# Kernel tuning notes

Hardware: AMD Instinct MI355X
Metric: run time of the kernel (lower is better)

The kernel has to match this reference:

```python
import jax, jax.numpy as jnp
import numpy as np

N_NODES = 50000
N_EDGES = 800000


def _sage(x, src, dst, Wl, Wr, b, n):
    # PyG SAGEConv: lin_l(mean aggr of neighbors) + lin_r(x) (+ bias in lin_l)
    agg = jax.ops.segment_sum(x[src], dst, num_segments=n)
    cnt = jax.ops.segment_sum(jnp.ones((src.shape[0],), x.dtype), dst, num_segments=n)
    mean = agg / jnp.maximum(cnt, 1.0)[:, None]
    return mean @ Wl + x @ Wr + b


def _gat(x, src, dst, W, att_src, att_dst, b, n):
    H, C = att_src.shape
    h = (x @ W).reshape(n, H, C)                      # [N,H,C]
    a_s = jnp.sum(h * att_src, axis=-1)               # [N,H]
    a_d = jnp.sum(h * att_dst, axis=-1)               # [N,H]
    e = jax.nn.leaky_relu(a_s[src] + a_d[dst], 0.2)   # [E,H]
    m = jax.ops.segment_max(e, dst, num_segments=n)   # per-dst softmax (stable)
    ex = jnp.exp(e - m[dst])
    s = jax.ops.segment_sum(ex, dst, num_segments=n)
    alpha = ex / (s[dst] + 1e-16)                     # [E,H]
    out = jax.ops.segment_sum(h[src] * alpha[:, :, None], dst, num_segments=n)
    return out.reshape(n, H * C) + b


def setup_inputs() -> dict:
    key = jax.random.key(0)
    ks = jax.random.split(key, 16)
    F_IN, H1, GH, HEADS, H2, NC = 20, 256, 32, 4, 256, 5
    GOUT = GH * HEADS
    sc = 0.05
    return {
        "x": jax.random.normal(ks[0], (N_NODES, F_IN), jnp.float32),
        "edge_index": jax.random.randint(ks[1], (2, N_EDGES), 0, N_NODES, jnp.int32),
        "sage1_Wl": jax.random.normal(ks[2], (F_IN, H1), jnp.float32) * sc,
        "sage1_Wr": jax.random.normal(ks[3], (F_IN, H1), jnp.float32) * sc,
        "sage1_b": jnp.zeros((H1,), jnp.float32),
        "gat_W": jax.random.normal(ks[4], (H1, GOUT), jnp.float32) * sc,
        "gat_att_src": jax.random.normal(ks[5], (HEADS, GH), jnp.float32) * sc,
        "gat_att_dst": jax.random.normal(ks[6], (HEADS, GH), jnp.float32) * sc,
        "gat_b": jnp.zeros((GOUT,), jnp.float32),
        "sage2_Wl": jax.random.normal(ks[7], (GOUT, H2), jnp.float32) * sc,
        "sage2_Wr": jax.random.normal(ks[8], (GOUT, H2), jnp.float32) * sc,
        "sage2_b": jnp.zeros((H2,), jnp.float32),
        "cls_W": jax.random.normal(ks[9], (H2, NC), jnp.float32) * sc,
        "cls_b": jnp.zeros((NC,), jnp.float32),
    }


def reference(x, edge_index, sage1_Wl, sage1_Wr, sage1_b, gat_W, gat_att_src,
              gat_att_dst, gat_b, sage2_Wl, sage2_Wr, sage2_b, cls_W, cls_b):
    n = x.shape[0]
    src, dst = edge_index[0], edge_index[1]
    h = jax.nn.relu(_sage(x, src, dst, sage1_Wl, sage1_Wr, sage1_b, n))
    h = jax.nn.elu(_gat(h, src, dst, gat_W, gat_att_src, gat_att_dst, gat_b, n))
    h = jax.nn.relu(_sage(h, src, dst, sage2_Wl, sage2_Wr, sage2_b, n))
    return h @ cls_W + cls_b
```

## Files before the change

kernel.cpp:

```cpp
#include <hip/hip_runtime.h>
#include <math.h>

#define N_NODES 50000
#define N_EDGES 800000
#define TPB 256
#define NCHUNK ((N_NODES + 255) / 256)

typedef short s16x8 __attribute__((ext_vector_type(8)));
typedef float f32x4 __attribute__((ext_vector_type(4)));

__device__ __forceinline__ unsigned short f2bf(float f) {
    unsigned u = __float_as_uint(f);
    u += 0x7fffu + ((u >> 16) & 1u);
    return (unsigned short)(u >> 16);
}
__device__ __forceinline__ float bf2f(unsigned short h) {
    return __uint_as_float(((unsigned)h) << 16);
}

__global__ void wt_k(const float* __restrict__ W1, int K1,
                     const float* __restrict__ W2, int K2,
                     int NO, int Kp, unsigned short* __restrict__ Wt) {
    int idx = blockIdx.x * TPB + threadIdx.x;
    if (idx >= NO * Kp) return;
    int n = idx / Kp, k = idx - n * Kp;
    float v = 0.f;
    if (k < K1) v = W1[(size_t)k * NO + n];
    else if (k < K1 + K2) v = W2[(size_t)(k - K1) * NO + n];
    Wt[idx] = f2bf(v);
}

__global__ void cast_k(const float4* __restrict__ in4, ushort4* __restrict__ outb) {
    int idx = blockIdx.x * TPB + threadIdx.x;
    if (idx >= N_NODES * 32) return;
    float4 v = in4[idx];
    ushort4 b;
    b.x = f2bf(v.x); b.y = f2bf(v.y); b.z = f2bf(v.z); b.w = f2bf(v.w);
    outb[idx] = b;
}

template<int ACT>
__global__ void gemm_mfma(const float* __restrict__ A1, int K1,
                          const float* __restrict__ A2, int K2,
                          const unsigned short* __restrict__ Wt, int Kp,
                          const float* __restrict__ bias,
                          float* __restrict__ out, int NO) {
    constexpr int BM = 128, BK = 32, LDP = 40;
    __shared__ unsigned short sA[BM * LDP];
    __shared__ unsigned short sB[128 * LDP];
    const int K = K1 + K2;
    const int T = Kp / BK;
    const int tid = threadIdx.x;
    const int lane = tid & 63, wid = tid >> 6;
    const int wr = wid >> 1, wc = wid & 1;
    const int row0 = blockIdx.y * BM, col0 = blockIdx.x * 128;
    const int l15 = lane & 15, l4 = lane >> 4;
    f32x4 acc[4][4] = {};

    for (int t = 0; t < T; ++t) {
        __syncthreads();
#pragma unroll
        for (int j = 0; j < 4; ++j) {
            int e = tid + j * 256;
            int r = e >> 3, k4 = e & 7;
            int kg = t * BK + k4 * 4, mg = row0 + r;
            float4 v = {0.f, 0.f, 0.f, 0.f};
            if (mg < N_NODES) {
                if (kg < K1)     v = *(const float4*)&A1[(size_t)mg * K1 + kg];
                else if (kg < K) v = *(const float4*)&A2[(size_t)mg * K2 + (kg - K1)];
            }
            ushort4 b;
            b.x = f2bf(v.x); b.y = f2bf(v.y); b.z = f2bf(v.z); b.w = f2bf(v.w);
            *(ushort4*)&sA[r * LDP + k4 * 4] = b;
        }
#pragma unroll
        for (int j = 0; j < 2; ++j) {
            int e = tid + j * 256;
            int n = e >> 2, k8 = e & 3;
            int4 v = *(const int4*)&Wt[(size_t)(col0 + n) * Kp + t * BK + k8 * 8];
            *(int4*)&sB[n * LDP + k8 * 8] = v;
        }
        __syncthreads();
        s16x8 af[4], bfr[4];
#pragma unroll
        for (int i = 0; i < 4; ++i) {
            af[i]  = *(const s16x8*)&sA[(wr * 64 + i * 16 + l15) * LDP + l4 * 8];
            bfr[i] = *(const s16x8*)&sB[(wc * 64 + i * 16 + l15) * LDP + l4 * 8];
        }
#pragma unroll
        for (int mi = 0; mi < 4; ++mi)
#pragma unroll
            for (int ni = 0; ni < 4; ++ni)
                acc[mi][ni] = __builtin_amdgcn_mfma_f32_16x16x32_bf16(
                    af[mi], bfr[ni], acc[mi][ni], 0, 0, 0);
    }
#pragma unroll
    for (int mi = 0; mi < 4; ++mi) {
#pragma unroll
        for (int ni = 0; ni < 4; ++ni) {
            int col = col0 + wc * 64 + ni * 16 + l15;
            float bb = bias ? bias[col] : 0.f;
#pragma unroll
            for (int r = 0; r < 4; ++r) {
                int row = row0 + wr * 64 + mi * 16 + l4 * 4 + r;
                if (row < N_NODES) {
                    float v = acc[mi][ni][r] + bb;
                    if (ACT) v = fmaxf(v, 0.f);
                    out[(size_t)row * NO + col] = v;
                }
            }
        }
    }
}

template<int ACT>
__global__ void gemm_mfma_bf(const unsigned short* __restrict__ A1, int K1,
                             const unsigned short* __restrict__ A2, int K2,
                             const unsigned short* __restrict__ Wt, int Kp,
                             const float* __restrict__ bias,
                             float* __restrict__ out, int NO) {
    constexpr int BM = 128, BK = 32, LDP = 40;
    __shared__ unsigned short sA[BM * LDP];
    __shared__ unsigned short sB[128 * LDP];
    const int T = Kp / BK;
    const int tid = threadIdx.x;
    const int lane = tid & 63, wid = tid >> 6;
    const int wr = wid >> 1, wc = wid & 1;
    const int row0 = blockIdx.y * BM, col0 = blockIdx.x * 128;
    const int l15 = lane & 15, l4 = lane >> 4;
    f32x4 acc[4][4] = {};

    for (int t = 0; t < T; ++t) {
        __syncthreads();
#pragma unroll
        for (int j = 0; j < 2; ++j) {
            int e = tid + j * 256;
            int r = e >> 2, k8 = e & 3;
            int kg = t * BK + k8 * 8, mg = row0 + r;
            int4 v = {0, 0, 0, 0};
            if (mg < N_NODES) {
                if (kg < K1) v = *(const int4*)&A1[(size_t)mg * K1 + kg];
                else         v = *(const int4*)&A2[(size_t)mg * K2 + (kg - K1)];
            }
            *(int4*)&sA[r * LDP + k8 * 8] = v;
        }
#pragma unroll
        for (int j = 0; j < 2; ++j) {
            int e = tid + j * 256;
            int n = e >> 2, k8 = e & 3;
            int4 v = *(const int4*)&Wt[(size_t)(col0 + n) * Kp + t * BK + k8 * 8];
            *(int4*)&sB[n * LDP + k8 * 8] = v;
        }
        __syncthreads();
        s16x8 af[4], bfr[4];
#pragma unroll
        for (int i = 0; i < 4; ++i) {
            af[i]  = *(const s16x8*)&sA[(wr * 64 + i * 16 + l15) * LDP + l4 * 8];
            bfr[i] = *(const s16x8*)&sB[(wc * 64 + i * 16 + l15) * LDP + l4 * 8];
        }
#pragma unroll
        for (int mi = 0; mi < 4; ++mi)
#pragma unroll
            for (int ni = 0; ni < 4; ++ni)
                acc[mi][ni] = __builtin_amdgcn_mfma_f32_16x16x32_bf16(
                    af[mi], bfr[ni], acc[mi][ni], 0, 0, 0);
    }
#pragma unroll
    for (int mi = 0; mi < 4; ++mi) {
#pragma unroll
        for (int ni = 0; ni < 4; ++ni) {
            int col = col0 + wc * 64 + ni * 16 + l15;
            float bb = bias ? bias[col] : 0.f;
#pragma unroll
            for (int r = 0; r < 4; ++r) {
                int row = row0 + wr * 64 + mi * 16 + l4 * 4 + r;
                if (row < N_NODES) {
                    float v = acc[mi][ni][r] + bb;
                    if (ACT) v = fmaxf(v, 0.f);
                    out[(size_t)row * NO + col] = v;
                }
            }
        }
    }
}

__global__ void hist_k(const int* __restrict__ dst, int* __restrict__ deg) {
    int e = blockIdx.x * TPB + threadIdx.x;
    if (e < N_EDGES) atomicAdd(&deg[dst[e]], 1);
}

__global__ void scan1_k(const int* __restrict__ deg, int* __restrict__ rowptr,
                        int* __restrict__ bsum) {
    __shared__ int tmp[256];
    int tid = threadIdx.x;
    int idx = blockIdx.x * 256 + tid;
    int v = (idx < N_NODES) ? deg[idx] : 0;
    tmp[tid] = v;
    __syncthreads();
    for (int off = 1; off < 256; off <<= 1) {
        int t = (tid >= off) ? tmp[tid - off] : 0;
        __syncthreads();
        tmp[tid] += t;
        __syncthreads();
    }
    if (idx < N_NODES) rowptr[idx] = tmp[tid] - v;
    if (tid == 255) bsum[blockIdx.x] = tmp[255];
}

__global__ void scan2_k(int* __restrict__ bsum) {
    __shared__ int tmp[256];
    int tid = threadIdx.x;
    int v = (tid < NCHUNK) ? bsum[tid] : 0;
    tmp[tid] = v;
    __syncthreads();
    for (int off = 1; off < 256; off <<= 1) {
        int t = (tid >= off) ? tmp[tid - off] : 0;
        __syncthreads();
        tmp[tid] += t;
        __syncthreads();
    }
    if (tid < NCHUNK) bsum[tid] = tmp[tid] - v;
}

__global__ void scan3_k(int* __restrict__ rowptr, const int* __restrict__ bsum) {
    int idx = blockIdx.x * 256 + threadIdx.x;
    if (idx < N_NODES) rowptr[idx] += bsum[blockIdx.x];
    if (idx == 0) rowptr[N_NODES] = N_EDGES;
}

__global__ void fill_k(const int* __restrict__ src, const int* __restrict__ dst,
                       const int* __restrict__ rowptr, int* __restrict__ deg,
                       int* __restrict__ csr_src) {
    int e = blockIdx.x * TPB + threadIdx.x;
    if (e >= N_EDGES) return;
    int d = dst[e];
    int r = atomicSub(&deg[d], 1) - 1;
    csr_src[rowptr[d] + r] = src[e];
}

template<int F, int BLK>
__global__ void gather_mean(const int* __restrict__ rowptr, const int* __restrict__ csr_src,
                            const float* __restrict__ feat, float* __restrict__ out) {
    int n = blockIdx.x;
    int c = threadIdx.x;
    if (c >= F) return;
    int e0 = rowptr[n], e1 = rowptr[n + 1];
    float acc = 0.f;
    for (int e = e0; e < e1; ++e)
        acc += feat[(size_t)csr_src[e] * F + c];
    out[(size_t)n * F + c] = acc / fmaxf((float)(e1 - e0), 1.0f);
}

__global__ void gather_mean_bf(const int* __restrict__ rowptr, const int* __restrict__ csr_src,
                               const unsigned short* __restrict__ featb,
                               unsigned short* __restrict__ outb) {
    int tid = threadIdx.x;
    int n = blockIdx.x * 8 + (tid >> 5);
    int c = tid & 31;
    int e0 = rowptr[n], e1 = rowptr[n + 1];
    float4 acc = {0.f, 0.f, 0.f, 0.f};
    int e = e0;
    for (; e + 1 < e1; e += 2) {
        int s0 = csr_src[e], s1 = csr_src[e + 1];
        ushort4 u0 = *(const ushort4*)&featb[(size_t)s0 * 128 + c * 4];
        ushort4 u1 = *(const ushort4*)&featb[(size_t)s1 * 128 + c * 4];
        acc.x += bf2f(u0.x) + bf2f(u1.x); acc.y += bf2f(u0.y) + bf2f(u1.y);
        acc.z += bf2f(u0.z) + bf2f(u1.z); acc.w += bf2f(u0.w) + bf2f(u1.w);
    }
    if (e < e1) {
        ushort4 u = *(const ushort4*)&featb[(size_t)csr_src[e] * 128 + c * 4];
        acc.x += bf2f(u.x); acc.y += bf2f(u.y); acc.z += bf2f(u.z); acc.w += bf2f(u.w);
    }
    float inv = 1.0f / fmaxf((float)(e1 - e0), 1.0f);
    ushort4 o;
    o.x = f2bf(acc.x * inv); o.y = f2bf(acc.y * inv);
    o.z = f2bf(acc.z * inv); o.w = f2bf(acc.w * inv);
    *(ushort4*)&outb[(size_t)n * 128 + c * 4] = o;
}

__global__ void att_scores(const float* __restrict__ h, const float* __restrict__ att_src,
                           const float* __restrict__ att_dst, float* __restrict__ as_,
                           float* __restrict__ ad_) {
    int idx = blockIdx.x * TPB + threadIdx.x;
    if (idx >= N_NODES * 4) return;
    int n = idx >> 2, hd = idx & 3;
    const float* row = h + (size_t)n * 128 + hd * 32;
    float sa = 0.f, sd = 0.f;
    for (int c = 0; c < 32; ++c) {
        float v = row[c];
        sa = fmaf(v, att_src[hd * 32 + c], sa);
        sd = fmaf(v, att_dst[hd * 32 + c], sd);
    }
    as_[idx] = sa;
    ad_[idx] = sd;
}

__global__ void gat_gather_bf(const int* __restrict__ rowptr, const int* __restrict__ csr_src,
                              const unsigned short* __restrict__ hb,
                              const float* __restrict__ as_, const float* __restrict__ ad_,
                              const float* __restrict__ gb,
                              unsigned short* __restrict__ outb) {
    int tid = threadIdx.x;
    int n = blockIdx.x * 8 + (tid >> 5);
    int c = tid & 31;
    int hd = c >> 3;
    int e0 = rowptr[n], e1 = rowptr[n + 1];
    float ad = ad_[n * 4 + hd];
    float m = -INFINITY, s = 0.f;
    float4 acc = {0.f, 0.f, 0.f, 0.f};
    int e = e0;
    for (; e + 1 < e1; e += 2) {
        int s0 = csr_src[e], s1 = csr_src[e + 1];
        float a0 = as_[s0 * 4 + hd] + ad;
        float a1 = as_[s1 * 4 + hd] + ad;
        a0 = a0 >= 0.f ? a0 : 0.2f * a0;
        a1 = a1 >= 0.f ? a1 : 0.2f * a1;
        float pm = fmaxf(a0, a1);
        if (pm > m) {
            float sc = __expf(m - pm);
            s *= sc; acc.x *= sc; acc.y *= sc; acc.z *= sc; acc.w *= sc;
            m = pm;
        }
        float ex0 = __expf(a0 - m), ex1 = __expf(a1 - m);
        s += ex0 + ex1;
        ushort4 u0 = *(const ushort4*)&hb[(size_t)s0 * 128 + c * 4];
        ushort4 u1 = *(const ushort4*)&hb[(size_t)s1 * 128 + c * 4];
        acc.x = fmaf(bf2f(u0.x), ex0, acc.x); acc.y = fmaf(bf2f(u0.y), ex0, acc.y);
        acc.z = fmaf(bf2f(u0.z), ex0, acc.z); acc.w = fmaf(bf2f(u0.w), ex0, acc.w);
        acc.x = fmaf(bf2f(u1.x), ex1, acc.x); acc.y = fmaf(bf2f(u1.y), ex1, acc.y);
        acc.z = fmaf(bf2f(u1.z), ex1, acc.z); acc.w = fmaf(bf2f(u1.w), ex1, acc.w);
    }
    if (e < e1) {
        int s0 = csr_src[e];
        float a = as_[s0 * 4 + hd] + ad;
        a = a >= 0.f ? a : 0.2f * a;
        if (a > m) {
            float sc = __expf(m - a);
            s *= sc; acc.x *= sc; acc.y *= sc; acc.z *= sc; acc.w *= sc;
            m = a;
        }
        float ex = __expf(a - m);
        s += ex;
        ushort4 u = *(const ushort4*)&hb[(size_t)s0 * 128 + c * 4];
        acc.x = fmaf(bf2f(u.x), ex, acc.x); acc.y = fmaf(bf2f(u.y), ex, acc.y);
        acc.z = fmaf(bf2f(u.z), ex, acc.z); acc.w = fmaf(bf2f(u.w), ex, acc.w);
    }
    float inv = 1.0f / (s + 1e-16f);
    float rx = acc.x * inv + gb[c * 4 + 0];
    float ry = acc.y * inv + gb[c * 4 + 1];
    float rz = acc.z * inv + gb[c * 4 + 2];
    float rw = acc.w * inv + gb[c * 4 + 3];
    rx = rx > 0.f ? rx : expm1f(rx);
    ry = ry > 0.f ? ry : expm1f(ry);
    rz = rz > 0.f ? rz : expm1f(rz);
    rw = rw > 0.f ? rw : expm1f(rw);
    ushort4 o;
    o.x = f2bf(rx); o.y = f2bf(ry); o.z = f2bf(rz); o.w = f2bf(rw);
    *(ushort4*)&outb[(size_t)n * 128 + c * 4] = o;
}

__global__ void cls_k(const float* __restrict__ h, const float* __restrict__ W,
                      const float* __restrict__ b, float* __restrict__ out) {
    __shared__ float sW[256 * 5];
    for (int i = threadIdx.x; i < 1280; i += TPB) sW[i] = W[i];
    __syncthreads();
    int n = blockIdx.x * TPB + threadIdx.x;
    if (n >= N_NODES) return;
    const float4* row = (const float4*)(h + (size_t)n * 256);
    float acc[5] = {0.f, 0.f, 0.f, 0.f, 0.f};
    for (int k4 = 0; k4 < 64; ++k4) {
        float4 v = row[k4];
        const float* w = &sW[k4 * 4 * 5];
#pragma unroll
        for (int c = 0; c < 5; ++c) acc[c] = fmaf(v.x, w[c], acc[c]);
#pragma unroll
        for (int c = 0; c < 5; ++c) acc[c] = fmaf(v.y, w[5 + c], acc[c]);
#pragma unroll
        for (int c = 0; c < 5; ++c) acc[c] = fmaf(v.z, w[10 + c], acc[c]);
#pragma unroll
        for (int c = 0; c < 5; ++c) acc[c] = fmaf(v.w, w[15 + c], acc[c]);
    }
#pragma unroll
    for (int c = 0; c < 5; ++c) out[(size_t)n * 5 + c] = acc[c] + b[c];
}

extern "C" void kernel_launch(void* const* d_in, const int* in_sizes, int n_in,
                              void* d_out, int out_size, void* d_ws, size_t ws_size,
                              hipStream_t stream) {
    const float* x    = (const float*)d_in[0];
    const int*   ei   = (const int*)d_in[1];
    const float* s1Wl = (const float*)d_in[2];
    const float* s1Wr = (const float*)d_in[3];
    const float* s1b  = (const float*)d_in[4];
    const float* gW   = (const float*)d_in[5];
    const float* gas  = (const float*)d_in[6];
    const float* gad  = (const float*)d_in[7];
    const float* gb   = (const float*)d_in[8];
    const float* s2Wl = (const float*)d_in[9];
    const float* s2Wr = (const float*)d_in[10];
    const float* s2b  = (const float*)d_in[11];
    const float* clsW = (const float*)d_in[12];
    const float* clsb = (const float*)d_in[13];
    float* out = (float*)d_out;
    const int* src = ei;
    const int* dst = ei + N_EDGES;

    float* ws  = (float*)d_ws;
    float* A   = ws;
    float* C   = A + (size_t)N_NODES * 256;
    float* as_ = C + (size_t)N_NODES * 128;
    float* ad_ = as_ + N_NODES * 4;
    int* deg     = (int*)(ad_ + N_NODES * 4);
    int* bsum    = deg + N_NODES;
    int* rowptr  = bsum + 256;
    int* csr_src = rowptr + N_NODES + 1;
    unsigned short* Wt1 = (unsigned short*)(csr_src + N_EDGES);
    unsigned short* Wt2 = Wt1 + 256 * 64;
    unsigned short* Wt3 = Wt2 + 128 * 256;
    unsigned short* Cb  = Wt3 + 256 * 256;
    unsigned short* Db  = Cb + (size_t)N_NODES * 128;
    unsigned short* Mb  = Db + (size_t)N_NODES * 128;

    const int MB = (N_NODES + 127) / 128;

    wt_k<<<(256 * 64 + TPB - 1) / TPB, TPB, 0, stream>>>(s1Wl, 20, s1Wr, 20, 256, 64, Wt1);
    wt_k<<<(128 * 256 + TPB - 1) / TPB, TPB, 0, stream>>>(gW, 256, nullptr, 0, 128, 256, Wt2);
    wt_k<<<(256 * 256 + TPB - 1) / TPB, TPB, 0, stream>>>(s2Wl, 128, s2Wr, 128, 256, 256, Wt3);

    hipMemsetAsync(deg, 0, N_NODES * sizeof(int), stream);
    hist_k<<<(N_EDGES + TPB - 1) / TPB, TPB, 0, stream>>>(dst, deg);
    scan1_k<<<NCHUNK, 256, 0, stream>>>(deg, rowptr, bsum);
    scan2_k<<<1, 256, 0, stream>>>(bsum);
    scan3_k<<<NCHUNK, 256, 0, stream>>>(rowptr, bsum);
    fill_k<<<(N_EDGES + TPB - 1) / TPB, TPB, 0, stream>>>(src, dst, rowptr, deg, csr_src);

    gather_mean<20, 64><<<N_NODES, 64, 0, stream>>>(rowptr, csr_src, x, C);
    gemm_mfma<1><<<dim3(2, MB), 256, 0, stream>>>(C, 20, x, 20, Wt1, 64, s1b, A, 256);

    gemm_mfma<0><<<dim3(1, MB), 256, 0, stream>>>(A, 256, nullptr, 0, Wt2, 256,
                                                  nullptr, C, 128);
    att_scores<<<(N_NODES * 4 + TPB - 1) / TPB, TPB, 0, stream>>>(C, gas, gad, as_, ad_);
    cast_k<<<(N_NODES * 32 + TPB - 1) / TPB, TPB, 0, stream>>>((const float4*)C,
                                                               (ushort4*)Cb);
    gat_gather_bf<<<N_NODES / 8, 256, 0, stream>>>(rowptr, csr_src, Cb, as_, ad_, gb, Db);

    gather_mean_bf<<<N_NODES / 8, 256, 0, stream>>>(rowptr, csr_src, Db, Mb);
    gemm_mfma_bf<1><<<dim3(2, MB), 256, 0, stream>>>(Mb, 128, Db, 128, Wt3, 256, s2b, A, 256);

    cls_k<<<(N_NODES + TPB - 1) / TPB, TPB, 0, stream>>>(A, clsW, clsb, out);
}
```

Measured before the change: 353.4 us.

## Emit bf16 from GEMM epilogues, merge weight prep, unroll gathers to four edges

The GEMM epilogues can now write bf16 directly. That removes the separate fp32-to-bf16 cast kernel and lets the GAT projection GEMM read bf16 input, halving the intermediate traffic. The three weight-transpose launches become one kernel. The first mean-gather now packs 8 nodes per block instead of one node per 64-thread block. The gather and attention loops unroll to four edges for more memory-level parallelism. Attention scores are computed from the bf16 features, which adds a little rounding error.

```diff
diff --git a/kernel.cpp b/kernel.cpp
--- a/kernel.cpp
+++ b/kernel.cpp
@@ -18,33 +18,36 @@
     return __uint_as_float(((unsigned)h) << 16);
 }
 
-__global__ void wt_k(const float* __restrict__ W1, int K1,
-                     const float* __restrict__ W2, int K2,
-                     int NO, int Kp, unsigned short* __restrict__ Wt) {
+__global__ void wt_all_k(const float* __restrict__ s1Wl, const float* __restrict__ s1Wr,
+                         const float* __restrict__ gW, const float* __restrict__ s2Wl,
+                         const float* __restrict__ s2Wr, unsigned short* __restrict__ Wt1,
+                         unsigned short* __restrict__ Wt2, unsigned short* __restrict__ Wt3) {
     int idx = blockIdx.x * TPB + threadIdx.x;
-    if (idx >= NO * Kp) return;
-    int n = idx / Kp, k = idx - n * Kp;
-    float v = 0.f;
-    if (k < K1) v = W1[(size_t)k * NO + n];
-    else if (k < K1 + K2) v = W2[(size_t)(k - K1) * NO + n];
-    Wt[idx] = f2bf(v);
-}
-
-__global__ void cast_k(const float4* __restrict__ in4, ushort4* __restrict__ outb) {
-    int idx = blockIdx.x * TPB + threadIdx.x;
-    if (idx >= N_NODES * 32) return;
-    float4 v = in4[idx];
-    ushort4 b;
-    b.x = f2bf(v.x); b.y = f2bf(v.y); b.z = f2bf(v.z); b.w = f2bf(v.w);
-    outb[idx] = b;
-}
-
-template<int ACT>
+    if (idx < 16384) {
+        int n = idx >> 6, k = idx & 63;
+        float v = 0.f;
+        if (k < 20) v = s1Wl[k * 256 + n];
+        else if (k < 40) v = s1Wr[(k - 20) * 256 + n];
+        Wt1[idx] = f2bf(v);
+    } else if (idx < 49152) {
+        int j = idx - 16384;
+        int n = j >> 8, k = j & 255;
+        Wt2[j] = f2bf(gW[(size_t)k * 128 + n]);
+    } else if (idx < 114688) {
+        int j = idx - 49152;
+        int n = j >> 8, k = j & 255;
+        float v = (k < 128) ? s2Wl[(size_t)k * 256 + n] : s2Wr[(size_t)(k - 128) * 256 + n];
+        Wt3[j] = f2bf(v);
+    }
+}
+
+template<int ACT, int OBF>
 __global__ void gemm_mfma(const float* __restrict__ A1, int K1,
                           const float* __restrict__ A2, int K2,
                           const unsigned short* __restrict__ Wt, int Kp,
                           const float* __restrict__ bias,
-                          float* __restrict__ out, int NO) {
+                          float* __restrict__ out, unsigned short* __restrict__ outb,
+                          int NO) {
     constexpr int BM = 128, BK = 32, LDP = 40;
     __shared__ unsigned short sA[BM * LDP];
     __shared__ unsigned short sB[128 * LDP];
@@ -106,19 +109,21 @@
                 if (row < N_NODES) {
                     float v = acc[mi][ni][r] + bb;
                     if (ACT) v = fmaxf(v, 0.f);
-                    out[(size_t)row * NO + col] = v;
+                    if (OBF) outb[(size_t)row * NO + col] = f2bf(v);
+                    else     out[(size_t)row * NO + col] = v;
                 }
             }
         }
     }
 }
 
-template<int ACT>
+template<int ACT, int OBF>
 __global__ void gemm_mfma_bf(const unsigned short* __restrict__ A1, int K1,
                              const unsigned short* __restrict__ A2, int K2,
                              const unsigned short* __restrict__ Wt, int Kp,
                              const float* __restrict__ bias,
-                             float* __restrict__ out, int NO) {
+                             float* __restrict__ out, unsigned short* __restrict__ outb,
+                             int NO) {
     constexpr int BM = 128, BK = 32, LDP = 40;
     __shared__ unsigned short sA[BM * LDP];
     __shared__ unsigned short sB[128 * LDP];
@@ -177,7 +182,8 @@
                 if (row < N_NODES) {
                     float v = acc[mi][ni][r] + bb;
                     if (ACT) v = fmaxf(v, 0.f);
-                    out[(size_t)row * NO + col] = v;
+                    if (OBF) outb[(size_t)row * NO + col] = f2bf(v);
+                    else     out[(size_t)row * NO + col] = v;
                 }
             }
         }
@@ -238,17 +244,20 @@
     csr_src[rowptr[d] + r] = src[e];
 }
 
-template<int F, int BLK>
-__global__ void gather_mean(const int* __restrict__ rowptr, const int* __restrict__ csr_src,
-                            const float* __restrict__ feat, float* __restrict__ out) {
-    int n = blockIdx.x;
-    int c = threadIdx.x;
-    if (c >= F) return;
+__global__ void gm20_k(const int* __restrict__ rowptr, const int* __restrict__ csr_src,
+                       const float* __restrict__ feat, float* __restrict__ out) {
+    int tid = threadIdx.x;
+    int n = blockIdx.x * 8 + (tid >> 5);
+    int c = tid & 31;
+    if (n >= N_NODES || c >= 20) return;
     int e0 = rowptr[n], e1 = rowptr[n + 1];
     float acc = 0.f;
-    for (int e = e0; e < e1; ++e)
-        acc += feat[(size_t)csr_src[e] * F + c];
-    out[(size_t)n * F + c] = acc / fmaxf((float)(e1 - e0), 1.0f);
+    int e = e0;
+    for (; e + 1 < e1; e += 2) {
+        acc += feat[(size_t)csr_src[e] * 20 + c] + feat[(size_t)csr_src[e + 1] * 20 + c];
+    }
+    if (e < e1) acc += feat[(size_t)csr_src[e] * 20 + c];
+    out[(size_t)n * 20 + c] = acc / fmaxf((float)(e1 - e0), 1.0f);
 }
 
 __global__ void gather_mean_bf(const int* __restrict__ rowptr, const int* __restrict__ csr_src,
@@ -260,14 +269,18 @@
     int e0 = rowptr[n], e1 = rowptr[n + 1];
     float4 acc = {0.f, 0.f, 0.f, 0.f};
     int e = e0;
-    for (; e + 1 < e1; e += 2) {
-        int s0 = csr_src[e], s1 = csr_src[e + 1];
+    for (; e + 3 < e1; e += 4) {
+        int s0 = csr_src[e], s1 = csr_src[e + 1], s2 = csr_src[e + 2], s3 = csr_src[e + 3];
         ushort4 u0 = *(const ushort4*)&featb[(size_t)s0 * 128 + c * 4];
         ushort4 u1 = *(const ushort4*)&featb[(size_t)s1 * 128 + c * 4];
-        acc.x += bf2f(u0.x) + bf2f(u1.x); acc.y += bf2f(u0.y) + bf2f(u1.y);
-        acc.z += bf2f(u0.z) + bf2f(u1.z); acc.w += bf2f(u0.w) + bf2f(u1.w);
-    }
-    if (e < e1) {
+        ushort4 u2 = *(const ushort4*)&featb[(size_t)s2 * 128 + c * 4];
+        ushort4 u3 = *(const ushort4*)&featb[(size_t)s3 * 128 + c * 4];
+        acc.x += (bf2f(u0.x) + bf2f(u1.x)) + (bf2f(u2.x) + bf2f(u3.x));
+        acc.y += (bf2f(u0.y) + bf2f(u1.y)) + (bf2f(u2.y) + bf2f(u3.y));
+        acc.z += (bf2f(u0.z) + bf2f(u1.z)) + (bf2f(u2.z) + bf2f(u3.z));
+        acc.w += (bf2f(u0.w) + bf2f(u1.w)) + (bf2f(u2.w) + bf2f(u3.w));
+    }
+    for (; e < e1; ++e) {
         ushort4 u = *(const ushort4*)&featb[(size_t)csr_src[e] * 128 + c * 4];
         acc.x += bf2f(u.x); acc.y += bf2f(u.y); acc.z += bf2f(u.z); acc.w += bf2f(u.w);
     }
@@ -278,18 +291,24 @@
     *(ushort4*)&outb[(size_t)n * 128 + c * 4] = o;
 }
 
-__global__ void att_scores(const float* __restrict__ h, const float* __restrict__ att_src,
-                           const float* __restrict__ att_dst, float* __restrict__ as_,
-                           float* __restrict__ ad_) {
+__global__ void att_scores_bf(const unsigned short* __restrict__ hb,
+                              const float* __restrict__ att_src,
+                              const float* __restrict__ att_dst,
+                              float* __restrict__ as_, float* __restrict__ ad_) {
     int idx = blockIdx.x * TPB + threadIdx.x;
     if (idx >= N_NODES * 4) return;
     int n = idx >> 2, hd = idx & 3;
-    const float* row = h + (size_t)n * 128 + hd * 32;
+    const unsigned short* row = hb + (size_t)n * 128 + hd * 32;
     float sa = 0.f, sd = 0.f;
-    for (int c = 0; c < 32; ++c) {
-        float v = row[c];
-        sa = fmaf(v, att_src[hd * 32 + c], sa);
-        sd = fmaf(v, att_dst[hd * 32 + c], sd);
+#pragma unroll
+    for (int c4 = 0; c4 < 8; ++c4) {
+        ushort4 u = *(const ushort4*)&row[c4 * 4];
+        const float* asr = &att_src[hd * 32 + c4 * 4];
+        const float* adr = &att_dst[hd * 32 + c4 * 4];
+        sa = fmaf(bf2f(u.x), asr[0], sa); sd = fmaf(bf2f(u.x), adr[0], sd);
+        sa = fmaf(bf2f(u.y), asr[1], sa); sd = fmaf(bf2f(u.y), adr[1], sd);
+        sa = fmaf(bf2f(u.z), asr[2], sa); sd = fmaf(bf2f(u.z), adr[2], sd);
+        sa = fmaf(bf2f(u.w), asr[3], sa); sd = fmaf(bf2f(u.w), adr[3], sd);
     }
     as_[idx] = sa;
     ad_[idx] = sd;
@@ -309,28 +328,39 @@
     float m = -INFINITY, s = 0.f;
     float4 acc = {0.f, 0.f, 0.f, 0.f};
     int e = e0;
-    for (; e + 1 < e1; e += 2) {
-        int s0 = csr_src[e], s1 = csr_src[e + 1];
+    for (; e + 3 < e1; e += 4) {
+        int s0 = csr_src[e], s1 = csr_src[e + 1], s2 = csr_src[e + 2], s3 = csr_src[e + 3];
         float a0 = as_[s0 * 4 + hd] + ad;
         float a1 = as_[s1 * 4 + hd] + ad;
+        float a2 = as_[s2 * 4 + hd] + ad;
+        float a3 = as_[s3 * 4 + hd] + ad;
         a0 = a0 >= 0.f ? a0 : 0.2f * a0;
         a1 = a1 >= 0.f ? a1 : 0.2f * a1;
-        float pm = fmaxf(a0, a1);
+        a2 = a2 >= 0.f ? a2 : 0.2f * a2;
+        a3 = a3 >= 0.f ? a3 : 0.2f * a3;
+        float pm = fmaxf(fmaxf(a0, a1), fmaxf(a2, a3));
         if (pm > m) {
             float sc = __expf(m - pm);
             s *= sc; acc.x *= sc; acc.y *= sc; acc.z *= sc; acc.w *= sc;
             m = pm;
         }
         float ex0 = __expf(a0 - m), ex1 = __expf(a1 - m);
-        s += ex0 + ex1;
+        float ex2 = __expf(a2 - m), ex3 = __expf(a3 - m);
+        s += (ex0 + ex1) + (ex2 + ex3);
         ushort4 u0 = *(const ushort4*)&hb[(size_t)s0 * 128 + c * 4];
         ushort4 u1 = *(const ushort4*)&hb[(size_t)s1 * 128 + c * 4];
+        ushort4 u2 = *(const ushort4*)&hb[(size_t)s2 * 128 + c * 4];
+        ushort4 u3 = *(const ushort4*)&hb[(size_t)s3 * 128 + c * 4];
         acc.x = fmaf(bf2f(u0.x), ex0, acc.x); acc.y = fmaf(bf2f(u0.y), ex0, acc.y);
         acc.z = fmaf(bf2f(u0.z), ex0, acc.z); acc.w = fmaf(bf2f(u0.w), ex0, acc.w);
         acc.x = fmaf(bf2f(u1.x), ex1, acc.x); acc.y = fmaf(bf2f(u1.y), ex1, acc.y);
         acc.z = fmaf(bf2f(u1.z), ex1, acc.z); acc.w = fmaf(bf2f(u1.w), ex1, acc.w);
-    }
-    if (e < e1) {
+        acc.x = fmaf(bf2f(u2.x), ex2, acc.x); acc.y = fmaf(bf2f(u2.y), ex2, acc.y);
+        acc.z = fmaf(bf2f(u2.z), ex2, acc.z); acc.w = fmaf(bf2f(u2.w), ex2, acc.w);
+        acc.x = fmaf(bf2f(u3.x), ex3, acc.x); acc.y = fmaf(bf2f(u3.y), ex3, acc.y);
+        acc.z = fmaf(bf2f(u3.z), ex3, acc.z); acc.w = fmaf(bf2f(u3.w), ex3, acc.w);
+    }
+    for (; e < e1; ++e) {
         int s0 = csr_src[e];
         float a = as_[s0 * 4 + hd] + ad;
         a = a >= 0.f ? a : 0.2f * a;
@@ -406,10 +436,10 @@
     const int* dst = ei + N_EDGES;
 
     float* ws  = (float*)d_ws;
-    float* A   = ws;
-    float* C   = A + (size_t)N_NODES * 256;
-    float* as_ = C + (size_t)N_NODES * 128;
-    float* ad_ = as_ + N_NODES * 4;
+    float* A    = ws;
+    float* M20  = A + (size_t)N_NODES * 256;
+    float* as_  = M20 + (size_t)N_NODES * 20;
+    float* ad_  = as_ + N_NODES * 4;
     int* deg     = (int*)(ad_ + N_NODES * 4);
     int* bsum    = deg + N_NODES;
     int* rowptr  = bsum + 256;
@@ -417,15 +447,15 @@
     unsigned short* Wt1 = (unsigned short*)(csr_src + N_EDGES);
     unsigned short* Wt2 = Wt1 + 256 * 64;
     unsigned short* Wt3 = Wt2 + 128 * 256;
-    unsigned short* Cb  = Wt3 + 256 * 256;
+    unsigned short* Ab  = Wt3 + 256 * 256;
+    unsigned short* Cb  = Ab + (size_t)N_NODES * 256;
     unsigned short* Db  = Cb + (size_t)N_NODES * 128;
     unsigned short* Mb  = Db + (size_t)N_NODES * 128;
 
     const int MB = (N_NODES + 127) / 128;
 
-    wt_k<<<(256 * 64 + TPB - 1) / TPB, TPB, 0, stream>>>(s1Wl, 20, s1Wr, 20, 256, 64, Wt1);
-    wt_k<<<(128 * 256 + TPB - 1) / TPB, TPB, 0, stream>>>(gW, 256, nullptr, 0, 128, 256, Wt2);
-    wt_k<<<(256 * 256 + TPB - 1) / TPB, TPB, 0, stream>>>(s2Wl, 128, s2Wr, 128, 256, 256, Wt3);
+    wt_all_k<<<(114688 + TPB - 1) / TPB, TPB, 0, stream>>>(s1Wl, s1Wr, gW, s2Wl, s2Wr,
+                                                           Wt1, Wt2, Wt3);
 
     hipMemsetAsync(deg, 0, N_NODES * sizeof(int), stream);
     hist_k<<<(N_EDGES + TPB - 1) / TPB, TPB, 0, stream>>>(dst, deg);
@@ -434,18 +464,18 @@
     scan3_k<<<NCHUNK, 256, 0, stream>>>(rowptr, bsum);
     fill_k<<<(N_EDGES + TPB - 1) / TPB, TPB, 0, stream>>>(src, dst, rowptr, deg, csr_src);
 
-    gather_mean<20, 64><<<N_NODES, 64, 0, stream>>>(rowptr, csr_src, x, C);
-    gemm_mfma<1><<<dim3(2, MB), 256, 0, stream>>>(C, 20, x, 20, Wt1, 64, s1b, A, 256);
-
-    gemm_mfma<0><<<dim3(1, MB), 256, 0, stream>>>(A, 256, nullptr, 0, Wt2, 256,
-                                                  nullptr, C, 128);
-    att_scores<<<(N_NODES * 4 + TPB - 1) / TPB, TPB, 0, stream>>>(C, gas, gad, as_, ad_);
-    cast_k<<<(N_NODES * 32 + TPB - 1) / TPB, TPB, 0, stream>>>((const float4*)C,
-                                                               (ushort4*)Cb);
+    gm20_k<<<(N_NODES + 7) / 8, 256, 0, stream>>>(rowptr, csr_src, x, M20);
+    gemm_mfma<1, 1><<<dim3(2, MB), 256, 0, stream>>>(M20, 20, x, 20, Wt1, 64, s1b,
+                                                     nullptr, Ab, 256);
+
+    gemm_mfma_bf<0, 1><<<dim3(1, MB), 256, 0, stream>>>(Ab, 256, nullptr, 0, Wt2, 256,
+                                                        nullptr, nullptr, Cb, 128);
+    att_scores_bf<<<(N_NODES * 4 + TPB - 1) / TPB, TPB, 0, stream>>>(Cb, gas, gad, as_, ad_);
     gat_gather_bf<<<N_NODES / 8, 256, 0, stream>>>(rowptr, csr_src, Cb, as_, ad_, gb, Db);
 
     gather_mean_bf<<<N_NODES / 8, 256, 0, stream>>>(rowptr, csr_src, Db, Mb);
-    gemm_mfma_bf<1><<<dim3(2, MB), 256, 0, stream>>>(Mb, 128, Db, 128, Wt3, 256, s2b, A, 256);
+    gemm_mfma_bf<1, 0><<<dim3(2, MB), 256, 0, stream>>>(Mb, 128, Db, 128, Wt3, 256, s2b,
+                                                        A, nullptr, 256);
 
     cls_k<<<(N_NODES + TPB - 1) / TPB, TPB, 0, stream>>>(A, clsW, clsb, out);
 }
```

Measured after the change: 296.0 us. 1.19x faster.
